# Optimization experiments

Measured on AMD Instinct MI355X. Metric: run time of the kernel, lower is better.

## Reference

```python
import jax, jax.numpy as jnp
import numpy as np

D_IN = 2048
NUM_HEADS = 32
NUM_KV = 8
HEAD_DIM = 64
V_HEAD_DIM = 64
SEQ = 2048
BATCH = 1
EPS = 1e-6
NEG = -1e30


def setup_inputs() -> dict:
    key = jax.random.key(0)
    ks = jax.random.split(key, 10)
    x = jax.random.normal(ks[0], (BATCH, SEQ, D_IN), dtype=jnp.float32)
    # causal mask: True = masked out (upper triangle above diagonal)
    mask = jnp.triu(jnp.ones((SEQ, SEQ), dtype=jnp.bool_), k=1)
    # RoPE tables
    inv_freq = 1.0 / (10000.0 ** (jnp.arange(0, HEAD_DIM, 2, dtype=jnp.float32) / HEAD_DIM))
    t = jnp.arange(SEQ, dtype=jnp.float32)
    freqs = jnp.outer(t, inv_freq)  # (S, hd/2)
    emb = jnp.concatenate([freqs, freqs], axis=-1)  # (S, hd)
    cos = jnp.cos(emb)
    sin = jnp.sin(emb)
    scale = 0.02
    wq = jax.random.normal(ks[1], (D_IN, NUM_HEADS * HEAD_DIM), dtype=jnp.float32) * scale
    wk = jax.random.normal(ks[2], (D_IN, NUM_KV * HEAD_DIM), dtype=jnp.float32) * scale
    wv = jax.random.normal(ks[3], (D_IN, NUM_KV * V_HEAD_DIM), dtype=jnp.float32) * scale
    wo = jax.random.normal(ks[4], (NUM_HEADS * V_HEAD_DIM, D_IN), dtype=jnp.float32) * scale
    q_norm_w = jnp.ones((HEAD_DIM,), dtype=jnp.float32)
    k_norm_w = jnp.ones((HEAD_DIM,), dtype=jnp.float32)
    sink = jax.random.normal(ks[5], (NUM_HEADS,), dtype=jnp.float32) * 0.02
    return {"x": x, "mask": mask, "cos": cos, "sin": sin, "wq": wq, "wk": wk,
            "wv": wv, "wo": wo, "q_norm_w": q_norm_w, "k_norm_w": k_norm_w, "sink": sink}


def _rmsnorm(x, w):
    var = jnp.mean(jnp.square(x), axis=-1, keepdims=True)
    return x * jax.lax.rsqrt(var + EPS) * w


def _rope(x, cos, sin):
    # x: (b, h, s, d); cos/sin: (s, d)
    d = x.shape[-1]
    x1, x2 = x[..., : d // 2], x[..., d // 2:]
    rot = jnp.concatenate([-x2, x1], axis=-1)
    return x * cos[None, None] + rot * sin[None, None]


def reference(x, mask, cos, sin, wq, wk, wv, wo, q_norm_w, k_norm_w, sink):
    b, s, _ = x.shape
    rep = NUM_HEADS // NUM_KV
    q = (x @ wq).reshape(b, s, NUM_HEADS, HEAD_DIM).transpose(0, 2, 1, 3)
    k = (x @ wk).reshape(b, s, NUM_KV, HEAD_DIM).transpose(0, 2, 1, 3)
    v = (x @ wv).reshape(b, s, NUM_KV, V_HEAD_DIM).transpose(0, 2, 1, 3)
    q = _rope(_rmsnorm(q, q_norm_w), cos, sin)
    k = _rope(_rmsnorm(k, k_norm_w), cos, sin)
    k = jnp.repeat(k, rep, axis=1)  # (b, H, s, hd)
    v = jnp.repeat(v, rep, axis=1)  # (b, H, s, vd)
    scores = jnp.einsum('bhqd,bhkd->bhqk', q, k) * (HEAD_DIM ** -0.5)
    scores = jnp.where(mask[:s, :s], NEG, scores)
    # append learnable sink logit per head
    sink_col = jnp.broadcast_to(sink.reshape(1, NUM_HEADS, 1, 1), (b, NUM_HEADS, s, 1))
    scores = jnp.concatenate([scores, sink_col], axis=-1)
    weights = jax.nn.softmax(scores, axis=-1)[..., :-1]  # drop sink column
    out = jnp.einsum('bhqk,bhkd->bhqd', weights, v)
    out = out.transpose(0, 2, 1, 3).reshape(b, s, NUM_HEADS * V_HEAD_DIM)
    return out @ wo
```

## Files before the change

### kernel.cpp

```cpp
#include <hip/hip_runtime.h>

typedef unsigned short u16;
typedef __bf16 bf16;
typedef float f32x4 __attribute__((ext_vector_type(4)));
typedef bf16 bf16x8 __attribute__((ext_vector_type(8)));
typedef short s16x4 __attribute__((ext_vector_type(4)));
typedef u16 u16x4 __attribute__((ext_vector_type(4)));
typedef u16 u16x8 __attribute__((ext_vector_type(8)));

#define SEQ 2048
#define LOG2E 1.4426950408889634f

__device__ __forceinline__ u16 f2bf(float f) {
    return __builtin_bit_cast(u16, (bf16)f);
}
__device__ __forceinline__ float bf2f(u16 u) {
    unsigned int w = ((unsigned int)u) << 16;
    return __builtin_bit_cast(float, w);
}

__global__ __launch_bounds__(256) void cast_bf16_k(const float* __restrict__ in,
                                                   u16* __restrict__ out, int n4) {
    int i = blockIdx.x * 256 + threadIdx.x;
    int stride = gridDim.x * 256;
    for (; i < n4; i += stride) {
        float4 v = reinterpret_cast<const float4*>(in)[i];
        u16x4 o;
        o[0] = f2bf(v.x); o[1] = f2bf(v.y); o[2] = f2bf(v.z); o[3] = f2bf(v.w);
        reinterpret_cast<u16x4*>(out)[i] = o;
    }
}

__global__ __launch_bounds__(256) void transpose_cast_k(const float* __restrict__ src,
                                                        u16* __restrict__ dst, int R, int C) {
    __shared__ float t[64][65];
    int c0 = blockIdx.x * 64, r0 = blockIdx.y * 64;
    int tx = threadIdx.x & 63, ty = threadIdx.x >> 6;
#pragma unroll
    for (int i = 0; i < 16; ++i) {
        int r = ty + i * 4;
        t[r][tx] = src[(size_t)(r0 + r) * C + c0 + tx];
    }
    __syncthreads();
#pragma unroll
    for (int i = 0; i < 16; ++i) {
        int c = ty + i * 4;
        dst[(size_t)(c0 + c) * R + r0 + tx] = f2bf(t[tx][c]);
    }
}

__global__ __launch_bounds__(256) void gemm_bt_dbuf_k(const u16* __restrict__ A,
                                                      const u16* __restrict__ Bt,
                                                      u16* __restrict__ Cp,
                                                      int M, int N, int K) {
    __shared__ __align__(16) u16 As[2][128 * 32];
    __shared__ __align__(16) u16 Bs[2][128 * 32];
    int tid = threadIdx.x;
    int wave = tid >> 6, lane = tid & 63;
    int bm = blockIdx.y * 128, bn = blockIdx.x * 128;
    int z = blockIdx.z;
    int kt0 = z * (K >> 1), ktend = kt0 + (K >> 1);
    int wm = (wave >> 1) * 64, wn = (wave & 1) * 64;
    int g = lane >> 4, cidx = lane & 15;
    f32x4 acc[4][4] = {};

    int srow = lane >> 2;
    int skol = ((lane & 3) ^ ((srow >> 1) & 3)) * 8;
    int sl8 = (g ^ ((cidx >> 1) & 3)) * 8;

#define STAGE(buf, kt)                                                                \
    {                                                                                 \
        _Pragma("unroll")                                                             \
        for (int j = 0; j < 2; ++j) {                                                 \
            const u16* gpa = A + (size_t)(bm + (wave * 2 + j) * 16 + srow) * K + (kt) + skol; \
            __builtin_amdgcn_global_load_lds(                                         \
                (__attribute__((address_space(1))) void*)gpa,                         \
                (__attribute__((address_space(3))) void*)&As[buf][(wave * 2 + j) * 512], \
                16, 0, 0);                                                            \
        }                                                                             \
        _Pragma("unroll")                                                             \
        for (int j = 0; j < 2; ++j) {                                                 \
            const u16* gpb = Bt + (size_t)(bn + (wave * 2 + j) * 16 + srow) * K + (kt) + skol; \
            __builtin_amdgcn_global_load_lds(                                         \
                (__attribute__((address_space(1))) void*)gpb,                         \
                (__attribute__((address_space(3))) void*)&Bs[buf][(wave * 2 + j) * 512], \
                16, 0, 0);                                                            \
        }                                                                             \
    }

    STAGE(0, kt0);
    asm volatile("s_waitcnt vmcnt(0)" ::: "memory");
    __syncthreads();

    int cur = 0;
#pragma unroll 1
    for (int kt = kt0; kt < ktend; kt += 32) {
        if (kt + 32 < ktend) STAGE(cur ^ 1, kt + 32);

        bf16x8 af[4], bfr[4];
#pragma unroll
        for (int mi = 0; mi < 4; ++mi)
            af[mi] = *reinterpret_cast<const bf16x8*>(&As[cur][(wm + mi * 16 + cidx) * 32 + sl8]);
#pragma unroll
        for (int ni = 0; ni < 4; ++ni)
            bfr[ni] = *reinterpret_cast<const bf16x8*>(&Bs[cur][(wn + ni * 16 + cidx) * 32 + sl8]);
#pragma unroll
        for (int mi = 0; mi < 4; ++mi)
#pragma unroll
            for (int ni = 0; ni < 4; ++ni)
                acc[mi][ni] = __builtin_amdgcn_mfma_f32_16x16x32_bf16(af[mi], bfr[ni], acc[mi][ni], 0, 0, 0);

        asm volatile("s_waitcnt vmcnt(0)" ::: "memory");
        __syncthreads();
        cur ^= 1;
    }
#undef STAGE

    u16* cbase = Cp + (size_t)z * M * N;
#pragma unroll
    for (int mi = 0; mi < 4; ++mi) {
#pragma unroll
        for (int r = 0; r < 4; ++r) {
            int row = bm + wm + mi * 16 + g * 4 + r;
            u16* cp = cbase + (size_t)row * N + bn + wn + cidx;
#pragma unroll
            for (int ni = 0; ni < 4; ++ni)
                cp[ni * 16] = f2bf(acc[mi][ni][r]);
        }
    }
}

__global__ __launch_bounds__(256) void sum2_f32_k(const u16* __restrict__ a,
                                                  const u16* __restrict__ b,
                                                  float* __restrict__ out, int n8) {
    int i = blockIdx.x * 256 + threadIdx.x;
    if (i >= n8) return;
    u16x8 va = reinterpret_cast<const u16x8*>(a)[i];
    u16x8 vb = reinterpret_cast<const u16x8*>(b)[i];
    f32x4 lo, hi;
#pragma unroll
    for (int j = 0; j < 4; ++j) {
        lo[j] = bf2f(va[j]) + bf2f(vb[j]);
        hi[j] = bf2f(va[4 + j]) + bf2f(vb[4 + j]);
    }
    reinterpret_cast<f32x4*>(out)[i * 2] = lo;
    reinterpret_cast<f32x4*>(out)[i * 2 + 1] = hi;
}

__global__ __launch_bounds__(256) void norm_rope_k(const u16* __restrict__ p0,
                                                   const u16* __restrict__ p1,
                                                   const float* __restrict__ cosb,
                                                   const float* __restrict__ sinb,
                                                   const float* __restrict__ qw,
                                                   const float* __restrict__ kw,
                                                   u16* __restrict__ qn,
                                                   u16* __restrict__ kfrag) {
    int idx = blockIdx.x * 4 + (threadIdx.x >> 6);
    int lane = threadIdx.x & 63;
    int s = idx / 40, hh = idx - s * 40;
    size_t off = (hh < 32) ? ((size_t)s * 3072 + hh * 64 + lane)
                           : ((size_t)s * 3072 + 2048 + (hh - 32) * 64 + lane);
    float val = bf2f(p0[off]) + bf2f(p1[off]);
    float ss = val * val;
#pragma unroll
    for (int mm = 32; mm; mm >>= 1) ss += __shfl_xor(ss, mm);
    float w = (hh < 32) ? qw[lane] : kw[lane];
    float xn = val * rsqrtf(ss * (1.f / 64.f) + 1e-6f) * w;
    float part = __shfl_xor(xn, 32);
    float rot = (lane < 32) ? -part : part;
    float o = xn * cosb[s * 64 + lane] + rot * sinb[s * 64 + lane];
    if (hh < 32) {
        qn[(size_t)s * 2048 + hh * 64 + lane] = f2bf(o * (0.125f * LOG2E));
    } else {
        int h8 = hh - 32;
        int k32 = s & 31;
        int p32 = ((k32 >> 2) & 1) * 16 + ((k32 >> 3) << 2) + (k32 & 3);
        int p = (s & ~31) + p32;
        kfrag[(((size_t)h8 * 128 + (p >> 4)) << 10) + (lane >> 3) * 128 + (p & 15) * 8 + (lane & 7)] = f2bf(o);
    }
}

__global__ __launch_bounds__(256) void v_frag_k(const u16* __restrict__ p0,
                                                const u16* __restrict__ p1,
                                                u16* __restrict__ vfrag) {
    __shared__ float t[64][65];
    int s0 = blockIdx.x * 64;
    int h = blockIdx.y;
    int tx = threadIdx.x & 63, ty = threadIdx.x >> 6;
#pragma unroll
    for (int i = 0; i < 16; ++i) {
        int r = ty + i * 4;
        size_t off = (size_t)(s0 + r) * 3072 + 2560 + h * 64 + tx;
        t[r][tx] = bf2f(p0[off]) + bf2f(p1[off]);
    }
    __syncthreads();
    int dt = threadIdx.x >> 6, g = (threadIdx.x >> 4) & 3, cc = threadIdx.x & 15;
#pragma unroll
    for (int kb = 0; kb < 2; ++kb) {
        u16x8 o;
#pragma unroll
        for (int i = 0; i < 8; ++i) o[i] = f2bf(t[kb * 32 + g * 8 + i][dt * 16 + cc]);
        *reinterpret_cast<u16x8*>(
            &vfrag[((size_t)h * 64 + (s0 >> 5) + kb) * 2048 + dt * 512 + (size_t)(threadIdx.x & 63) * 8]) = o;
    }
}

__global__ __launch_bounds__(256, 4) void attn_k(const u16* __restrict__ qn,
                                                 const u16* __restrict__ kfrag,
                                                 const u16* __restrict__ vfrag,
                                                 u16* __restrict__ obuf,
                                                 float* __restrict__ lbuf) {
    int kvh = blockIdx.x;
    int wave = threadIdx.x >> 6, lane = threadIdx.x & 63;
    int h = kvh * 4 + wave;
    int j = 319 - blockIdx.y;
    int c, w;
    if (j < 32)       { c = j;                    w = 0; }
    else if (j < 96)  { c = 32 + ((j - 32) >> 1); w = (j - 32) & 1; }
    else if (j < 192) { int r = j - 96;  int q = r / 3; c = 64 + q; w = r - 3 * q; }
    else              { c = 96 + ((j - 192) >> 2); w = (j - 192) & 3; }

    int q0 = c * 16;
    int nk = q0 + 16;
    int kv0 = w * 512;
    int kvend = (kv0 + 512 < nk) ? (kv0 + 512) : nk;

    int g = lane >> 4, cc = lane & 15;
    int qrow = q0 + cc;

    const size_t qoff = (size_t)qrow * 2048 + h * 64;
    bf16x8 q_0 = *reinterpret_cast<const bf16x8*>(&qn[qoff + g * 8]);
    bf16x8 q_1 = *reinterpret_cast<const bf16x8*>(&qn[qoff + 32 + g * 8]);

    float l = 0.f;
    f32x4 o[4] = {};

    const u16* kbase = kfrag + (((size_t)kvh * 128) << 10) + lane * 8;
    const u16* vbase = vfrag + (size_t)kvh * 64 * 2048 + lane * 8;

    bf16x8 kf0[4], kf1[4];
#pragma unroll
    for (int sub = 0; sub < 4; ++sub) {
        const u16* kp = kbase + (size_t)((kv0 >> 4) + sub) * 1024;
        kf0[sub] = *reinterpret_cast<const bf16x8*>(kp);
        kf1[sub] = *reinterpret_cast<const bf16x8*>(kp + 512);
    }

#pragma unroll 1
    for (; kv0 < kvend; kv0 += 64) {
        __builtin_amdgcn_s_barrier();

        f32x4 st[4];
        __builtin_amdgcn_s_setprio(1);
#pragma unroll
        for (int sub = 0; sub < 4; ++sub) {
            st[sub] = __builtin_amdgcn_mfma_f32_16x16x32_bf16(kf0[sub], q_0, (f32x4){0.f, 0.f, 0.f, 0.f}, 0, 0, 0);
            st[sub] = __builtin_amdgcn_mfma_f32_16x16x32_bf16(kf1[sub], q_1, st[sub], 0, 0, 0);
        }
        __builtin_amdgcn_s_setprio(0);

        if (kv0 + 64 < kvend) {
#pragma unroll
            for (int sub = 0; sub < 4; ++sub) {
                const u16* kp = kbase + (size_t)(((kv0 + 64) >> 4) + sub) * 1024;
                kf0[sub] = *reinterpret_cast<const bf16x8*>(kp);
                kf1[sub] = *reinterpret_cast<const bf16x8*>(kp + 512);
            }
        }

        bf16x8 vv[2][4];
#pragma unroll
        for (int sp = 0; sp < 2; ++sp)
#pragma unroll
            for (int dt = 0; dt < 4; ++dt)
                vv[sp][dt] = *reinterpret_cast<const bf16x8*>(
                    vbase + (size_t)((kv0 >> 5) + sp) * 2048 + dt * 512);

        if (kv0 + 64 > q0) {
#pragma unroll
            for (int sub = 0; sub < 4; ++sub)
#pragma unroll
                for (int r = 0; r < 4; ++r) {
                    int key = kv0 + (sub >> 1) * 32 + g * 8 + (sub & 1) * 4 + r;
                    if (key > qrow) st[sub][r] = -1e30f;
                }
        }

        u16x8 pb[2];
        float rs = 0.f;
#pragma unroll
        for (int sub = 0; sub < 4; ++sub)
#pragma unroll
            for (int r = 0; r < 4; ++r) {
                float e = __builtin_amdgcn_exp2f(st[sub][r]);
                rs += e;
                pb[sub >> 1][(sub & 1) * 4 + r] = f2bf(e);
            }
        l += rs;

        __builtin_amdgcn_s_setprio(1);
#pragma unroll
        for (int sp = 0; sp < 2; ++sp) {
            bf16x8 pbb = __builtin_bit_cast(bf16x8, pb[sp]);
#pragma unroll
            for (int dt = 0; dt < 4; ++dt)
                o[dt] = __builtin_amdgcn_mfma_f32_16x16x32_bf16(vv[sp][dt], pbb, o[dt], 0, 0, 0);
        }
        __builtin_amdgcn_s_setprio(0);
    }

    l += __shfl_xor(l, 16);
    l += __shfl_xor(l, 32);
    size_t slot = (size_t)h * 320 + j;
    if (lane < 16) lbuf[slot * 16 + cc] = l;
    u16* sp = obuf + slot * 1024;
#pragma unroll
    for (int dt = 0; dt < 4; ++dt) {
        u16x4 ov;
#pragma unroll
        for (int r = 0; r < 4; ++r) ov[r] = f2bf(o[dt][r]);
        *reinterpret_cast<u16x4*>(&sp[cc * 64 + dt * 16 + g * 4]) = ov;
    }
}

__global__ __launch_bounds__(256) void merge_k(const u16* __restrict__ obuf,
                                               const float* __restrict__ lbuf,
                                               const float* __restrict__ sink,
                                               u16* __restrict__ attnb) {
    int row = blockIdx.x;
    int c = row >> 4, cc = row & 15;
    int nw = (c >> 5) + 1;
    int jb = (c < 32) ? c
           : (c < 64) ? 32 + ((c - 32) << 1)
           : (c < 96) ? 96 + 3 * (c - 64)
                      : 192 + ((c - 96) << 2);
    int t = threadIdx.x;
    int h = t >> 3, col0 = (t & 7) * 8;

    float acc[8] = {};
    float lsum = __builtin_amdgcn_exp2f(sink[h] * LOG2E);
#pragma unroll 1
    for (int w = 0; w < nw; ++w) {
        size_t slot = (size_t)h * 320 + jb + w;
        lsum += lbuf[slot * 16 + cc];
        u16x8 v = *reinterpret_cast<const u16x8*>(&obuf[slot * 1024 + cc * 64 + col0]);
#pragma unroll
        for (int i = 0; i < 8; ++i) acc[i] += bf2f(v[i]);
    }
    float inv = 1.f / lsum;
    u16x8 ob;
#pragma unroll
    for (int i = 0; i < 8; ++i) ob[i] = f2bf(acc[i] * inv);
    *reinterpret_cast<u16x8*>(&attnb[(size_t)row * 2048 + h * 64 + col0]) = ob;
}

extern "C" void kernel_launch(void* const* d_in, const int* in_sizes, int n_in,
                              void* d_out, int out_size, void* d_ws, size_t ws_size,
                              hipStream_t stream) {
    const float* x    = (const float*)d_in[0];
    const float* cosb = (const float*)d_in[2];
    const float* sinb = (const float*)d_in[3];
    const float* wq   = (const float*)d_in[4];
    const float* wk   = (const float*)d_in[5];
    const float* wv   = (const float*)d_in[6];
    const float* wo   = (const float*)d_in[7];
    const float* qw   = (const float*)d_in[8];
    const float* kw   = (const float*)d_in[9];
    const float* sink = (const float*)d_in[10];
    float* out = (float*)d_out;

    char* ws = (char*)d_ws;
    size_t off = 0;
    auto alloc = [&](size_t bytes) {
        char* p = ws + off;
        off += (bytes + 255) & ~(size_t)255;
        return p;
    };
    u16*   xb    = (u16*)alloc((size_t)2048 * 2048 * 2);
    u16*   wqkvt = (u16*)alloc((size_t)3072 * 2048 * 2);
    u16*   wot   = (u16*)alloc((size_t)2048 * 2048 * 2);
    u16*   p0    = (u16*)alloc((size_t)2048 * 3072 * 2);
    u16*   p1    = (u16*)alloc((size_t)2048 * 3072 * 2);
    u16*   qnb   = (u16*)alloc((size_t)2048 * 2048 * 2);
    u16*   kfrag = (u16*)alloc((size_t)8 * 128 * 1024 * 2);
    u16*   vfrag = (u16*)alloc((size_t)8 * 64 * 2048 * 2);
    float* lbuf  = (float*)alloc((size_t)32 * 320 * 16 * 4);
    u16*   attnb = xb;
    u16*   obuf  = p0;
    u16*   o2p   = p0;

    cast_bf16_k<<<2048, 256, 0, stream>>>(x, xb, 2048 * 2048 / 4);
    transpose_cast_k<<<dim3(32, 32), 256, 0, stream>>>(wq, wqkvt, 2048, 2048);
    transpose_cast_k<<<dim3(8, 32), 256, 0, stream>>>(wk, wqkvt + (size_t)2048 * 2048, 2048, 512);
    transpose_cast_k<<<dim3(8, 32), 256, 0, stream>>>(wv, wqkvt + (size_t)2560 * 2048, 2048, 512);
    transpose_cast_k<<<dim3(32, 32), 256, 0, stream>>>(wo, wot, 2048, 2048);

    gemm_bt_dbuf_k<<<dim3(24, 16, 2), 256, 0, stream>>>(xb, wqkvt, p0, 2048, 3072, 2048);
    norm_rope_k<<<20480, 256, 0, stream>>>(p0, p1, cosb, sinb, qw, kw, qnb, kfrag);
    v_frag_k<<<dim3(32, 8), 256, 0, stream>>>(p0, p1, vfrag);

    attn_k<<<dim3(8, 320), 256, 0, stream>>>(qnb, kfrag, vfrag, obuf, lbuf);
    merge_k<<<2048, 256, 0, stream>>>(obuf, lbuf, sink, attnb);

    gemm_bt_dbuf_k<<<dim3(16, 16, 2), 256, 0, stream>>>(attnb, wot, o2p, 2048, 2048, 2048);
    sum2_f32_k<<<2048, 256, 0, stream>>>(o2p, o2p + (size_t)2048 * 2048, out, 2048 * 2048 / 8);
}
```

Measured before the change: 163.9 us.

## Process two 16-row query tiles per wave to reuse K/V fragments

Each wave in the attention kernel now handles two adjacent 16-row query tiles (32 rows) instead of one, so every loaded K and V fragment feeds two sets of MFMAs. The grid is halved to 160 work items, and the merge kernel's slot indexing is updated to the new pairing. The per-iteration barrier is removed and V loads are moved ahead of the QK MFMAs to start them earlier. This cuts global/L2 K/V traffic per FLOP and increases ILP, at the cost of more registers (which may pressure the launch bound of 4 blocks/SM) and fewer blocks for load balancing. Tile A also does some extra masked work on its diagonal block.

```diff
diff --git a/kernel.cpp b/kernel.cpp
--- a/kernel.cpp
+++ b/kernel.cpp
@@ -213,27 +213,31 @@
     int kvh = blockIdx.x;
     int wave = threadIdx.x >> 6, lane = threadIdx.x & 63;
     int h = kvh * 4 + wave;
-    int j = 319 - blockIdx.y;
-    int c, w;
-    if (j < 32)       { c = j;                    w = 0; }
-    else if (j < 96)  { c = 32 + ((j - 32) >> 1); w = (j - 32) & 1; }
-    else if (j < 192) { int r = j - 96;  int q = r / 3; c = 64 + q; w = r - 3 * q; }
-    else              { c = 96 + ((j - 192) >> 2); w = (j - 192) & 3; }
-
-    int q0 = c * 16;
-    int nk = q0 + 16;
+    int item = 159 - blockIdx.y;
+    int t, w;
+    if (item < 16)      { t = item;                   w = 0; }
+    else if (item < 48) { t = 16 + ((item - 16) >> 1); w = (item - 16) & 1; }
+    else if (item < 96) { int r = item - 48; int q = r / 3; t = 32 + q; w = r - 3 * q; }
+    else                { t = 48 + ((item - 96) >> 2); w = (item - 96) & 3; }
+
+    int qA0 = t * 32;
+    int qB0 = qA0 + 16;
     int kv0 = w * 512;
-    int kvend = (kv0 + 512 < nk) ? (kv0 + 512) : nk;
+    int nkB = qB0 + 16;
+    int kvend = (kv0 + 512 < nkB) ? (kv0 + 512) : nkB;
 
     int g = lane >> 4, cc = lane & 15;
-    int qrow = q0 + cc;
-
-    const size_t qoff = (size_t)qrow * 2048 + h * 64;
-    bf16x8 q_0 = *reinterpret_cast<const bf16x8*>(&qn[qoff + g * 8]);
-    bf16x8 q_1 = *reinterpret_cast<const bf16x8*>(&qn[qoff + 32 + g * 8]);
-
-    float l = 0.f;
-    f32x4 o[4] = {};
+    int qrowA = qA0 + cc, qrowB = qB0 + cc;
+
+    const size_t qoffA = (size_t)qrowA * 2048 + h * 64;
+    const size_t qoffB = (size_t)qrowB * 2048 + h * 64;
+    bf16x8 qa0 = *reinterpret_cast<const bf16x8*>(&qn[qoffA + g * 8]);
+    bf16x8 qa1 = *reinterpret_cast<const bf16x8*>(&qn[qoffA + 32 + g * 8]);
+    bf16x8 qb0 = *reinterpret_cast<const bf16x8*>(&qn[qoffB + g * 8]);
+    bf16x8 qb1 = *reinterpret_cast<const bf16x8*>(&qn[qoffB + 32 + g * 8]);
+
+    float lA = 0.f, lB = 0.f;
+    f32x4 oA[4] = {}, oB[4] = {};
 
     const u16* kbase = kfrag + (((size_t)kvh * 128) << 10) + lane * 8;
     const u16* vbase = vfrag + (size_t)kvh * 64 * 2048 + lane * 8;
@@ -248,14 +252,22 @@
 
 #pragma unroll 1
     for (; kv0 < kvend; kv0 += 64) {
-        __builtin_amdgcn_s_barrier();
-
-        f32x4 st[4];
+        bf16x8 vv[2][4];
+#pragma unroll
+        for (int sp = 0; sp < 2; ++sp)
+#pragma unroll
+            for (int dt = 0; dt < 4; ++dt)
+                vv[sp][dt] = *reinterpret_cast<const bf16x8*>(
+                    vbase + (size_t)((kv0 >> 5) + sp) * 2048 + dt * 512);
+
+        f32x4 stA[4], stB[4];
         __builtin_amdgcn_s_setprio(1);
 #pragma unroll
         for (int sub = 0; sub < 4; ++sub) {
-            st[sub] = __builtin_amdgcn_mfma_f32_16x16x32_bf16(kf0[sub], q_0, (f32x4){0.f, 0.f, 0.f, 0.f}, 0, 0, 0);
-            st[sub] = __builtin_amdgcn_mfma_f32_16x16x32_bf16(kf1[sub], q_1, st[sub], 0, 0, 0);
+            stA[sub] = __builtin_amdgcn_mfma_f32_16x16x32_bf16(kf0[sub], qa0, (f32x4){0.f, 0.f, 0.f, 0.f}, 0, 0, 0);
+            stB[sub] = __builtin_amdgcn_mfma_f32_16x16x32_bf16(kf0[sub], qb0, (f32x4){0.f, 0.f, 0.f, 0.f}, 0, 0, 0);
+            stA[sub] = __builtin_amdgcn_mfma_f32_16x16x32_bf16(kf1[sub], qa1, stA[sub], 0, 0, 0);
+            stB[sub] = __builtin_amdgcn_mfma_f32_16x16x32_bf16(kf1[sub], qb1, stB[sub], 0, 0, 0);
         }
         __builtin_amdgcn_s_setprio(0);
 
@@ -268,58 +280,68 @@
             }
         }
 
-        bf16x8 vv[2][4];
-#pragma unroll
-        for (int sp = 0; sp < 2; ++sp)
-#pragma unroll
-            for (int dt = 0; dt < 4; ++dt)
-                vv[sp][dt] = *reinterpret_cast<const bf16x8*>(
-                    vbase + (size_t)((kv0 >> 5) + sp) * 2048 + dt * 512);
-
-        if (kv0 + 64 > q0) {
+        if (kv0 + 64 > qA0) {
 #pragma unroll
             for (int sub = 0; sub < 4; ++sub)
 #pragma unroll
                 for (int r = 0; r < 4; ++r) {
                     int key = kv0 + (sub >> 1) * 32 + g * 8 + (sub & 1) * 4 + r;
-                    if (key > qrow) st[sub][r] = -1e30f;
+                    if (key > qrowA) stA[sub][r] = -1e30f;
+                    if (key > qrowB) stB[sub][r] = -1e30f;
                 }
         }
 
-        u16x8 pb[2];
-        float rs = 0.f;
+        u16x8 pbA[2], pbB[2];
+        float rsA = 0.f, rsB = 0.f;
 #pragma unroll
         for (int sub = 0; sub < 4; ++sub)
 #pragma unroll
             for (int r = 0; r < 4; ++r) {
-                float e = __builtin_amdgcn_exp2f(st[sub][r]);
-                rs += e;
-                pb[sub >> 1][(sub & 1) * 4 + r] = f2bf(e);
+                float eA = __builtin_amdgcn_exp2f(stA[sub][r]);
+                float eB = __builtin_amdgcn_exp2f(stB[sub][r]);
+                rsA += eA;
+                rsB += eB;
+                pbA[sub >> 1][(sub & 1) * 4 + r] = f2bf(eA);
+                pbB[sub >> 1][(sub & 1) * 4 + r] = f2bf(eB);
             }
-        l += rs;
+        lA += rsA;
+        lB += rsB;
 
         __builtin_amdgcn_s_setprio(1);
 #pragma unroll
         for (int sp = 0; sp < 2; ++sp) {
-            bf16x8 pbb = __builtin_bit_cast(bf16x8, pb[sp]);
-#pragma unroll
-            for (int dt = 0; dt < 4; ++dt)
-                o[dt] = __builtin_amdgcn_mfma_f32_16x16x32_bf16(vv[sp][dt], pbb, o[dt], 0, 0, 0);
+            bf16x8 pa = __builtin_bit_cast(bf16x8, pbA[sp]);
+            bf16x8 pb = __builtin_bit_cast(bf16x8, pbB[sp]);
+#pragma unroll
+            for (int dt = 0; dt < 4; ++dt) {
+                oA[dt] = __builtin_amdgcn_mfma_f32_16x16x32_bf16(vv[sp][dt], pa, oA[dt], 0, 0, 0);
+                oB[dt] = __builtin_amdgcn_mfma_f32_16x16x32_bf16(vv[sp][dt], pb, oB[dt], 0, 0, 0);
+            }
         }
         __builtin_amdgcn_s_setprio(0);
     }
 
-    l += __shfl_xor(l, 16);
-    l += __shfl_xor(l, 32);
-    size_t slot = (size_t)h * 320 + j;
-    if (lane < 16) lbuf[slot * 16 + cc] = l;
-    u16* sp = obuf + slot * 1024;
+    lA += __shfl_xor(lA, 16);
+    lA += __shfl_xor(lA, 32);
+    lB += __shfl_xor(lB, 16);
+    lB += __shfl_xor(lB, 32);
+    size_t slotA = ((size_t)h * 160 + item) * 2;
+    if (lane < 16) {
+        lbuf[slotA * 16 + cc] = lA;
+        lbuf[(slotA + 1) * 16 + cc] = lB;
+    }
+    u16* spA = obuf + slotA * 1024;
+    u16* spB = obuf + (slotA + 1) * 1024;
 #pragma unroll
     for (int dt = 0; dt < 4; ++dt) {
-        u16x4 ov;
-#pragma unroll
-        for (int r = 0; r < 4; ++r) ov[r] = f2bf(o[dt][r]);
-        *reinterpret_cast<u16x4*>(&sp[cc * 64 + dt * 16 + g * 4]) = ov;
+        u16x4 ovA, ovB;
+#pragma unroll
+        for (int r = 0; r < 4; ++r) {
+            ovA[r] = f2bf(oA[dt][r]);
+            ovB[r] = f2bf(oB[dt][r]);
+        }
+        *reinterpret_cast<u16x4*>(&spA[cc * 64 + dt * 16 + g * 4]) = ovA;
+        *reinterpret_cast<u16x4*>(&spB[cc * 64 + dt * 16 + g * 4]) = ovB;
     }
 }
 
@@ -329,11 +351,12 @@
                                                u16* __restrict__ attnb) {
     int row = blockIdx.x;
     int c = row >> 4, cc = row & 15;
-    int nw = (c >> 5) + 1;
-    int jb = (c < 32) ? c
-           : (c < 64) ? 32 + ((c - 32) << 1)
-           : (c < 96) ? 96 + 3 * (c - 64)
-                      : 192 + ((c - 96) << 2);
+    int t2 = c >> 1, half = c & 1;
+    int nw = (t2 >> 4) + 1;
+    int jb = (t2 < 16) ? t2
+           : (t2 < 32) ? 16 + ((t2 - 16) << 1)
+           : (t2 < 48) ? 48 + 3 * (t2 - 32)
+                       : 96 + ((t2 - 48) << 2);
     int t = threadIdx.x;
     int h = t >> 3, col0 = (t & 7) * 8;
 
@@ -341,7 +364,7 @@
     float lsum = __builtin_amdgcn_exp2f(sink[h] * LOG2E);
 #pragma unroll 1
     for (int w = 0; w < nw; ++w) {
-        size_t slot = (size_t)h * 320 + jb + w;
+        size_t slot = ((size_t)h * 160 + jb + w) * 2 + half;
         lsum += lbuf[slot * 16 + cc];
         u16x8 v = *reinterpret_cast<const u16x8*>(&obuf[slot * 1024 + cc * 64 + col0]);
 #pragma unroll
@@ -399,7 +422,7 @@
     norm_rope_k<<<20480, 256, 0, stream>>>(p0, p1, cosb, sinb, qw, kw, qnb, kfrag);
     v_frag_k<<<dim3(32, 8), 256, 0, stream>>>(p0, p1, vfrag);
 
-    attn_k<<<dim3(8, 320), 256, 0, stream>>>(qnb, kfrag, vfrag, obuf, lbuf);
+    attn_k<<<dim3(8, 160), 256, 0, stream>>>(qnb, kfrag, vfrag, obuf, lbuf);
     merge_k<<<2048, 256, 0, stream>>>(obuf, lbuf, sink, attnb);
 
     gemm_bt_dbuf_k<<<dim3(16, 16, 2), 256, 0, stream>>>(attnb, wot, o2p, 2048, 2048, 2048);
```

Measured after the change: 241.2 us. +47.2%, slower.

## Drop split-KV partitioning and merge kernel, normalize attention output in-kernel

Applied to the files above, without the earlier changes.

Removes the split-KV decomposition (320 work items per head with up to 4 KV splits) and the separate merge kernel. Each block now processes a full 16-row query chunk across the whole causal key range and writes the normalized output, including the sink term, directly to the attention buffer. V fragment loads are also moved to the top of the loop so they are issued before the QK MFMAs. This eliminates the partial-output round trip through global memory and one kernel launch, but reduces parallelism to 1024 blocks with highly unbalanced work, since the longest block covers 2048 keys.

```diff
diff --git a/kernel.cpp b/kernel.cpp
--- a/kernel.cpp
+++ b/kernel.cpp
@@ -208,22 +208,14 @@
 __global__ __launch_bounds__(256, 4) void attn_k(const u16* __restrict__ qn,
                                                  const u16* __restrict__ kfrag,
                                                  const u16* __restrict__ vfrag,
-                                                 u16* __restrict__ obuf,
-                                                 float* __restrict__ lbuf) {
+                                                 const float* __restrict__ sink,
+                                                 u16* __restrict__ attnb) {
     int kvh = blockIdx.x;
     int wave = threadIdx.x >> 6, lane = threadIdx.x & 63;
     int h = kvh * 4 + wave;
-    int j = 319 - blockIdx.y;
-    int c, w;
-    if (j < 32)       { c = j;                    w = 0; }
-    else if (j < 96)  { c = 32 + ((j - 32) >> 1); w = (j - 32) & 1; }
-    else if (j < 192) { int r = j - 96;  int q = r / 3; c = 64 + q; w = r - 3 * q; }
-    else              { c = 96 + ((j - 192) >> 2); w = (j - 192) & 3; }
-
+    int c = 127 - blockIdx.y;
     int q0 = c * 16;
-    int nk = q0 + 16;
-    int kv0 = w * 512;
-    int kvend = (kv0 + 512 < nk) ? (kv0 + 512) : nk;
+    int kvend = q0 + 16;
 
     int g = lane >> 4, cc = lane & 15;
     int qrow = q0 + cc;
@@ -241,14 +233,22 @@
     bf16x8 kf0[4], kf1[4];
 #pragma unroll
     for (int sub = 0; sub < 4; ++sub) {
-        const u16* kp = kbase + (size_t)((kv0 >> 4) + sub) * 1024;
+        const u16* kp = kbase + (size_t)sub * 1024;
         kf0[sub] = *reinterpret_cast<const bf16x8*>(kp);
         kf1[sub] = *reinterpret_cast<const bf16x8*>(kp + 512);
     }
 
 #pragma unroll 1
-    for (; kv0 < kvend; kv0 += 64) {
+    for (int kv0 = 0; kv0 < kvend; kv0 += 64) {
         __builtin_amdgcn_s_barrier();
+
+        bf16x8 vv[2][4];
+#pragma unroll
+        for (int sp = 0; sp < 2; ++sp)
+#pragma unroll
+            for (int dt = 0; dt < 4; ++dt)
+                vv[sp][dt] = *reinterpret_cast<const bf16x8*>(
+                    vbase + (size_t)((kv0 >> 5) + sp) * 2048 + dt * 512);
 
         f32x4 st[4];
         __builtin_amdgcn_s_setprio(1);
@@ -267,14 +267,6 @@
                 kf1[sub] = *reinterpret_cast<const bf16x8*>(kp + 512);
             }
         }
-
-        bf16x8 vv[2][4];
-#pragma unroll
-        for (int sp = 0; sp < 2; ++sp)
-#pragma unroll
-            for (int dt = 0; dt < 4; ++dt)
-                vv[sp][dt] = *reinterpret_cast<const bf16x8*>(
-                    vbase + (size_t)((kv0 >> 5) + sp) * 2048 + dt * 512);
 
         if (kv0 + 64 > q0) {
 #pragma unroll
@@ -311,47 +303,14 @@
 
     l += __shfl_xor(l, 16);
     l += __shfl_xor(l, 32);
-    size_t slot = (size_t)h * 320 + j;
-    if (lane < 16) lbuf[slot * 16 + cc] = l;
-    u16* sp = obuf + slot * 1024;
+    float inv = 1.f / (l + __builtin_amdgcn_exp2f(sink[h] * LOG2E));
 #pragma unroll
     for (int dt = 0; dt < 4; ++dt) {
         u16x4 ov;
 #pragma unroll
-        for (int r = 0; r < 4; ++r) ov[r] = f2bf(o[dt][r]);
-        *reinterpret_cast<u16x4*>(&sp[cc * 64 + dt * 16 + g * 4]) = ov;
-    }
-}
-
-__global__ __launch_bounds__(256) void merge_k(const u16* __restrict__ obuf,
-                                               const float* __restrict__ lbuf,
-                                               const float* __restrict__ sink,
-                                               u16* __restrict__ attnb) {
-    int row = blockIdx.x;
-    int c = row >> 4, cc = row & 15;
-    int nw = (c >> 5) + 1;
-    int jb = (c < 32) ? c
-           : (c < 64) ? 32 + ((c - 32) << 1)
-           : (c < 96) ? 96 + 3 * (c - 64)
-                      : 192 + ((c - 96) << 2);
-    int t = threadIdx.x;
-    int h = t >> 3, col0 = (t & 7) * 8;
-
-    float acc[8] = {};
-    float lsum = __builtin_amdgcn_exp2f(sink[h] * LOG2E);
-#pragma unroll 1
-    for (int w = 0; w < nw; ++w) {
-        size_t slot = (size_t)h * 320 + jb + w;
-        lsum += lbuf[slot * 16 + cc];
-        u16x8 v = *reinterpret_cast<const u16x8*>(&obuf[slot * 1024 + cc * 64 + col0]);
-#pragma unroll
-        for (int i = 0; i < 8; ++i) acc[i] += bf2f(v[i]);
-    }
-    float inv = 1.f / lsum;
-    u16x8 ob;
-#pragma unroll
-    for (int i = 0; i < 8; ++i) ob[i] = f2bf(acc[i] * inv);
-    *reinterpret_cast<u16x8*>(&attnb[(size_t)row * 2048 + h * 64 + col0]) = ob;
+        for (int r = 0; r < 4; ++r) ov[r] = f2bf(o[dt][r] * inv);
+        *reinterpret_cast<u16x4*>(&attnb[(size_t)qrow * 2048 + h * 64 + dt * 16 + g * 4]) = ov;
+    }
 }
 
 extern "C" void kernel_launch(void* const* d_in, const int* in_sizes, int n_in,
@@ -384,9 +343,7 @@
     u16*   qnb   = (u16*)alloc((size_t)2048 * 2048 * 2);
     u16*   kfrag = (u16*)alloc((size_t)8 * 128 * 1024 * 2);
     u16*   vfrag = (u16*)alloc((size_t)8 * 64 * 2048 * 2);
-    float* lbuf  = (float*)alloc((size_t)32 * 320 * 16 * 4);
     u16*   attnb = xb;
-    u16*   obuf  = p0;
     u16*   o2p   = p0;
 
     cast_bf16_k<<<2048, 256, 0, stream>>>(x, xb, 2048 * 2048 / 4);
@@ -399,8 +356,7 @@
     norm_rope_k<<<20480, 256, 0, stream>>>(p0, p1, cosb, sinb, qw, kw, qnb, kfrag);
     v_frag_k<<<dim3(32, 8), 256, 0, stream>>>(p0, p1, vfrag);
 
-    attn_k<<<dim3(8, 320), 256, 0, stream>>>(qnb, kfrag, vfrag, obuf, lbuf);
-    merge_k<<<2048, 256, 0, stream>>>(obuf, lbuf, sink, attnb);
+    attn_k<<<dim3(8, 128), 256, 0, stream>>>(qnb, kfrag, vfrag, sink, attnb);
 
     gemm_bt_dbuf_k<<<dim3(16, 16, 2), 256, 0, stream>>>(attnb, wot, o2p, 2048, 2048, 2048);
     sum2_f32_k<<<2048, 256, 0, stream>>>(o2p, o2p + (size_t)2048 * 2048, out, 2048 * 2048 / 8);
```

Result: faster. 153.9 us (-6.1%).
